# Optimization experiments

Hardware: AMD Instinct MI355X
Metric: run time of the kernel (lower is better)

Reference implementation:

```python
import jax, jax.numpy as jnp
import numpy as np

B, D_IN, D_H = 8192, 1024, 1024

def setup_inputs() -> dict:
    key = jax.random.key(0)
    ks = jax.random.split(key, 20)
    s_in = 1.0 / np.sqrt(D_IN)
    s_h = 1.0 / np.sqrt(D_H)
    inp = {
        'input': jax.random.normal(ks[0], (B, D_IN), jnp.float32),
        'h_0': jax.random.normal(ks[1], (B, D_H), jnp.float32),
        'c_0': jax.random.normal(ks[2], (B, D_H), jnp.float32),
    }
    names = ['i', 'f', 'g', 'o']
    for idx, g in enumerate(names):
        inp[f'W_{g}_i2h'] = jax.random.uniform(ks[3 + 4 * idx], (D_H, D_IN), jnp.float32, -s_in, s_in)
        inp[f'b_{g}_i2h'] = jax.random.uniform(ks[4 + 4 * idx], (D_H,), jnp.float32, -s_in, s_in)
        inp[f'W_{g}_h2h'] = jax.random.uniform(ks[5 + 4 * idx], (D_H, D_H), jnp.float32, -s_h, s_h)
        inp[f'b_{g}_h2h'] = jax.random.uniform(ks[6 + 4 * idx], (D_H,), jnp.float32, -s_h, s_h)
    return inp


def reference(input, h_0, c_0,
              W_i_i2h, b_i_i2h, W_i_h2h, b_i_h2h,
              W_f_i2h, b_f_i2h, W_f_h2h, b_f_h2h,
              W_g_i2h, b_g_i2h, W_g_h2h, b_g_h2h,
              W_o_i2h, b_o_i2h, W_o_h2h, b_o_h2h):
    # pre-activations: x @ W_i2h^T + b + h @ W_h2h^T + b  (Linear uses y = x W^T + b)
    def lin(x, W, b):
        return x @ W.T + b
    it = jax.nn.sigmoid(lin(input, W_i_i2h, b_i_i2h) + lin(h_0, W_i_h2h, b_i_h2h))
    ft = jax.nn.sigmoid(lin(input, W_f_i2h, b_f_i2h) + lin(h_0, W_f_h2h, b_f_h2h))
    ot = jax.nn.sigmoid(lin(input, W_o_i2h, b_o_i2h) + lin(h_0, W_o_h2h, b_o_h2h))
    gt = jnp.tanh(lin(input, W_g_i2h, b_g_i2h) + lin(h_0, W_g_h2h, b_g_h2h))
    ct = ft * c_0 + it * gt
    output = ot * jnp.tanh(ct)
    return (output, ct)
```

## Files before the change

### kernel.cpp

```cpp
#include <hip/hip_runtime.h>
#include <cstdint>

typedef __attribute__((ext_vector_type(8))) short bf16x8;
typedef __attribute__((ext_vector_type(4))) float f32x4;
typedef __attribute__((ext_vector_type(8))) unsigned short u16x8;

typedef __attribute__((address_space(1))) unsigned int gu32_t;
typedef __attribute__((address_space(3))) unsigned int lu32_t;

#define BATCH 8192
#define DIN 1024
#define DH 1024
#define KD 2048
#define ND 4096

__device__ __forceinline__ unsigned short f2bf(float f) {
    union { float f; unsigned int u; } v; v.f = f;
    unsigned int u = v.u;
    u += 0x7fffu + ((u >> 16) & 1u);
    return (unsigned short)(u >> 16);
}
__device__ __forceinline__ float sigmoidf_(float x) {
    return 1.0f / (1.0f + __expf(-x));
}
__device__ __forceinline__ float tanhf_(float x) {
    float xc = fminf(fmaxf(x, -15.0f), 15.0f);
    float e2 = __expf(2.0f * xc);
    return (e2 - 1.0f) / (e2 + 1.0f);
}

__global__ void __launch_bounds__(256) convert_all(
        const float* __restrict__ x, const float* __restrict__ h,
        const float* __restrict__ Wii, const float* __restrict__ Wih,
        const float* __restrict__ Wfi, const float* __restrict__ Wfh,
        const float* __restrict__ Wgi, const float* __restrict__ Wgh,
        const float* __restrict__ Woi, const float* __restrict__ Woh,
        const float* __restrict__ bii, const float* __restrict__ bih,
        const float* __restrict__ bfi, const float* __restrict__ bfh,
        const float* __restrict__ bgi, const float* __restrict__ bgh,
        const float* __restrict__ boi, const float* __restrict__ boh,
        unsigned short* __restrict__ A, unsigned short* __restrict__ B,
        float* __restrict__ bsum) {
    const int t = blockIdx.x * 256 + threadIdx.x;
    if (t < 2097152) {
        const int64_t off = (int64_t)t * 8;
        const int row = (int)(off >> 11);
        const int k = (int)(off & 2047);
        const float* src = (k < DIN) ? (x + (int64_t)row * DIN + k)
                                     : (h + (int64_t)row * DH + (k - DIN));
        f32x4 v0 = *(const f32x4*)src;
        f32x4 v1 = *(const f32x4*)(src + 4);
        u16x8 o;
        o[0] = f2bf(v0[0]); o[1] = f2bf(v0[1]); o[2] = f2bf(v0[2]); o[3] = f2bf(v0[3]);
        o[4] = f2bf(v1[0]); o[5] = f2bf(v1[1]); o[6] = f2bf(v1[2]); o[7] = f2bf(v1[3]);
        *(u16x8*)(A + off) = o;
    } else if (t < 3145728) {
        const int tb = t - 2097152;
        const int64_t off = (int64_t)tb * 8;
        const int brow = (int)(off >> 11);
        const int k = (int)(off & 2047);
        const int gate = brow & 3;
        const int n = brow >> 2;
        const float* Wi2h = (gate == 0) ? Wii : (gate == 1) ? Wfi : (gate == 2) ? Wgi : Woi;
        const float* Wh2h = (gate == 0) ? Wih : (gate == 1) ? Wfh : (gate == 2) ? Wgh : Woh;
        const float* src = (k < 1024) ? (Wi2h + (int64_t)n * 1024 + k)
                                      : (Wh2h + (int64_t)n * 1024 + (k - 1024));
        f32x4 v0 = *(const f32x4*)src;
        f32x4 v1 = *(const f32x4*)(src + 4);
        u16x8 o;
        o[0] = f2bf(v0[0]); o[1] = f2bf(v0[1]); o[2] = f2bf(v0[2]); o[3] = f2bf(v0[3]);
        o[4] = f2bf(v1[0]); o[5] = f2bf(v1[1]); o[6] = f2bf(v1[2]); o[7] = f2bf(v1[3]);
        *(u16x8*)(B + off) = o;
    } else {
        const int b = t - 3145728;
#pragma unroll
        for (int i = 0; i < 8; ++i) {
            const int e = b * 8 + i;
            const int n = e >> 2;
            const int g = e & 3;
            const float* bi = (g == 0) ? bii : (g == 1) ? bfi : (g == 2) ? bgi : boi;
            const float* bh = (g == 0) ? bih : (g == 1) ? bfh : (g == 2) ? bgh : boh;
            bsum[e] = bi[n] + bh[n];
        }
    }
}

__global__ void __launch_bounds__(256) gemm_lstm(
        const unsigned short* __restrict__ A,
        const unsigned short* __restrict__ Bw,
        const float* __restrict__ c0,
        const float* __restrict__ bsum,
        float* __restrict__ out) {
    __shared__ __align__(16) unsigned short ldsA[128 * 32];
    __shared__ __align__(16) unsigned short ldsB[128 * 32];
    __shared__ __align__(16) float preLds[64][128];

    const int bid = blockIdx.x;
    const int swz = ((bid & 7) << 8) | (bid >> 3);
    const int bm = swz >> 5;
    const int bn = swz & 31;
    const int t = threadIdx.x;
    const int lane = t & 63;
    const int wave = t >> 6;
    const int wm = (wave >> 1) << 6;
    const int wn = (wave & 1) << 6;

    f32x4 acc[4][4];
#pragma unroll
    for (int m = 0; m < 4; ++m)
#pragma unroll
        for (int n = 0; n < 4; ++n)
            acc[m][n] = (f32x4){0.f, 0.f, 0.f, 0.f};

    const int c0i = t;
    const int c1i = t + 256;
    const int64_t aOff0 = (int64_t)(bm * 128 + (c0i >> 2)) * KD + ((c0i & 3) << 3);
    const int64_t aOff1 = (int64_t)(bm * 128 + (c1i >> 2)) * KD + ((c1i & 3) << 3);
    const int64_t bOff0 = (int64_t)(bn * 128 + (c0i >> 2)) * KD + ((c0i & 3) << 3);
    const int64_t bOff1 = (int64_t)(bn * 128 + (c1i >> 2)) * KD + ((c1i & 3) << 3);
    unsigned short* lA0 = &ldsA[wave * 512];
    unsigned short* lA1 = &ldsA[2048 + wave * 512];
    unsigned short* lB0 = &ldsB[wave * 512];
    unsigned short* lB1 = &ldsB[2048 + wave * 512];

    const int r = lane & 15;
    const int kq = (lane >> 4) << 3;

    for (int k0 = 0; k0 < KD; k0 += 32) {
        __syncthreads();
        __builtin_amdgcn_global_load_lds((const gu32_t*)(A + aOff0 + k0), (lu32_t*)lA0, 16, 0, 0);
        __builtin_amdgcn_global_load_lds((const gu32_t*)(A + aOff1 + k0), (lu32_t*)lA1, 16, 0, 0);
        __builtin_amdgcn_global_load_lds((const gu32_t*)(Bw + bOff0 + k0), (lu32_t*)lB0, 16, 0, 0);
        __builtin_amdgcn_global_load_lds((const gu32_t*)(Bw + bOff1 + k0), (lu32_t*)lB1, 16, 0, 0);
        __syncthreads();

        bf16x8 af[4], bfr[4];
#pragma unroll
        for (int m = 0; m < 4; ++m)
            af[m] = *(const bf16x8*)&ldsA[(wm + m * 16 + r) * 32 + kq];
#pragma unroll
        for (int n = 0; n < 4; ++n)
            bfr[n] = *(const bf16x8*)&ldsB[(wn + n * 16 + r) * 32 + kq];
#pragma unroll
        for (int m = 0; m < 4; ++m)
#pragma unroll
            for (int n = 0; n < 4; ++n)
                acc[m][n] = __builtin_amdgcn_mfma_f32_16x16x32_bf16(af[m], bfr[n], acc[m][n], 0, 0, 0);
    }

    f32x4 bs[4];
#pragma unroll
    for (int i = 0; i < 4; ++i)
        bs[i] = *(const f32x4*)&bsum[bn * 128 + (t & 7) * 16 + i * 4];

    const int rq = (lane >> 4) << 2;

#pragma unroll
    for (int c = 0; c < 2; ++c) {
        __syncthreads();
        if (wm == c * 64) {
#pragma unroll
            for (int m = 0; m < 4; ++m)
#pragma unroll
                for (int n = 0; n < 4; ++n)
#pragma unroll
                    for (int j = 0; j < 4; ++j)
                        preLds[m * 16 + rq + j][wn + n * 16 + r] = acc[m][n][j];
        }
        __syncthreads();
#pragma unroll
        for (int p = 0; p < 2; ++p) {
            const int lr = p * 32 + (t >> 3);
            const int R = bm * 128 + c * 64 + lr;
            f32x4 pr[4];
#pragma unroll
            for (int i = 0; i < 4; ++i)
                pr[i] = *(const f32x4*)&preLds[lr][(t & 7) * 16 + i * 4];
            const int64_t eo = (int64_t)R * DH + bn * 32 + (t & 7) * 4;
            f32x4 cv = *(const f32x4*)&c0[eo];
            f32x4 hv, ctv;
#pragma unroll
            for (int j = 0; j < 4; ++j) {
                float it = sigmoidf_(pr[j][0] + bs[j][0]);
                float ft = sigmoidf_(pr[j][1] + bs[j][1]);
                float gt = tanhf_(pr[j][2] + bs[j][2]);
                float ot = sigmoidf_(pr[j][3] + bs[j][3]);
                float ct = ft * cv[j] + it * gt;
                ctv[j] = ct;
                hv[j] = ot * tanhf_(ct);
            }
            *(f32x4*)&out[eo] = hv;
            *(f32x4*)&out[(int64_t)BATCH * DH + eo] = ctv;
        }
    }
}

extern "C" void kernel_launch(void* const* d_in, const int* in_sizes, int n_in,
                              void* d_out, int out_size, void* d_ws, size_t ws_size,
                              hipStream_t stream) {
    const float* x   = (const float*)d_in[0];
    const float* h0  = (const float*)d_in[1];
    const float* c0  = (const float*)d_in[2];
    const float* Wii = (const float*)d_in[3];
    const float* bii = (const float*)d_in[4];
    const float* Wih = (const float*)d_in[5];
    const float* bih = (const float*)d_in[6];
    const float* Wfi = (const float*)d_in[7];
    const float* bfi = (const float*)d_in[8];
    const float* Wfh = (const float*)d_in[9];
    const float* bfh = (const float*)d_in[10];
    const float* Wgi = (const float*)d_in[11];
    const float* bgi = (const float*)d_in[12];
    const float* Wgh = (const float*)d_in[13];
    const float* bgh = (const float*)d_in[14];
    const float* Woi = (const float*)d_in[15];
    const float* boi = (const float*)d_in[16];
    const float* Woh = (const float*)d_in[17];
    const float* boh = (const float*)d_in[18];

    unsigned short* A  = (unsigned short*)d_ws;
    unsigned short* Bw = A + (size_t)BATCH * KD;
    float* bsum = (float*)(Bw + (size_t)ND * KD);
    float* out = (float*)d_out;

    convert_all<<<12290, 256, 0, stream>>>(x, h0,
        Wii, Wih, Wfi, Wfh, Wgi, Wgh, Woi, Woh,
        bii, bih, bfi, bfh, bgi, bgh, boi, boh,
        A, Bw, bsum);
    gemm_lstm<<<2048, 256, 0, stream>>>(A, Bw, c0, bsum, out);
}
```

Baseline: 406.5 us.

## Use 256x256 tiles, 4-stage LDS pipeline, and XOR-swizzled shared memory in LSTM GEMM

The GEMM now uses 256x256 block tiles with 8 waves (512 threads) and a 4-buffer LDS ring. Global-to-LDS loads are issued three k-steps ahead, with explicit vmcnt waits and a single barrier per step, so memory latency overlaps with MFMA work. LDS reads and the epilogue staging buffer use an XOR swizzle to cut bank conflicts, and MFMA sections raise wave priority with s_setprio. The larger tiles improve data reuse per loaded byte. In exchange there are fewer blocks (512), higher register pressure from 32 accumulators per thread, and 128KB of LDS per block.

```diff
diff --git a/kernel.cpp b/kernel.cpp
--- a/kernel.cpp
+++ b/kernel.cpp
@@ -27,6 +27,9 @@
     float xc = fminf(fmaxf(x, -15.0f), 15.0f);
     float e2 = __expf(2.0f * xc);
     return (e2 - 1.0f) / (e2 + 1.0f);
+}
+__device__ __forceinline__ int fswz(int r) {
+    return ((r & 3) << 4) ^ ((r & 4) << 3);
 }
 
 __global__ void __launch_bounds__(256) convert_all(
@@ -85,113 +88,148 @@
     }
 }
 
-__global__ void __launch_bounds__(256) gemm_lstm(
+__global__ void __launch_bounds__(512, 2) gemm_lstm(
         const unsigned short* __restrict__ A,
         const unsigned short* __restrict__ Bw,
-        const float* __restrict__ c0,
+        const float* __restrict__ c0p,
         const float* __restrict__ bsum,
-        float* __restrict__ out) {
-    __shared__ __align__(16) unsigned short ldsA[128 * 32];
-    __shared__ __align__(16) unsigned short ldsB[128 * 32];
-    __shared__ __align__(16) float preLds[64][128];
+        float* __restrict__ outp) {
+    __shared__ __align__(16) unsigned short lds[4][16384];
 
     const int bid = blockIdx.x;
-    const int swz = ((bid & 7) << 8) | (bid >> 3);
-    const int bm = swz >> 5;
-    const int bn = swz & 31;
+    const int swz = ((bid & 7) << 6) | (bid >> 3);
+    const int bm = swz & 31;
+    const int bn = swz >> 5;
     const int t = threadIdx.x;
     const int lane = t & 63;
     const int wave = t >> 6;
-    const int wm = (wave >> 1) << 6;
-    const int wn = (wave & 1) << 6;
-
-    f32x4 acc[4][4];
-#pragma unroll
-    for (int m = 0; m < 4; ++m)
+    const int wm = wave >> 2;
+    const int wn = wave & 3;
+
+    f32x4 acc[8][4];
+#pragma unroll
+    for (int m = 0; m < 8; ++m)
 #pragma unroll
         for (int n = 0; n < 4; ++n)
             acc[m][n] = (f32x4){0.f, 0.f, 0.f, 0.f};
 
-    const int c0i = t;
-    const int c1i = t + 256;
-    const int64_t aOff0 = (int64_t)(bm * 128 + (c0i >> 2)) * KD + ((c0i & 3) << 3);
-    const int64_t aOff1 = (int64_t)(bm * 128 + (c1i >> 2)) * KD + ((c1i & 3) << 3);
-    const int64_t bOff0 = (int64_t)(bn * 128 + (c0i >> 2)) * KD + ((c0i & 3) << 3);
-    const int64_t bOff1 = (int64_t)(bn * 128 + (c1i >> 2)) * KD + ((c1i & 3) << 3);
-    unsigned short* lA0 = &ldsA[wave * 512];
-    unsigned short* lA1 = &ldsA[2048 + wave * 512];
-    unsigned short* lB0 = &ldsB[wave * 512];
-    unsigned short* lB1 = &ldsB[2048 + wave * 512];
-
-    const int r = lane & 15;
-    const int kq = (lane >> 4) << 3;
-
-    for (int k0 = 0; k0 < KD; k0 += 32) {
+    const int crow = t >> 2;
+    const int kb = ((t & 3) << 4) ^ fswz(crow & 7);
+    const unsigned short* aS0 = A  + (size_t)(bm * 256 + crow) * KD + (kb >> 1);
+    const unsigned short* aS1 = aS0 + (size_t)128 * KD;
+    const unsigned short* bS0 = Bw + (size_t)(bn * 256 + crow) * KD + (kb >> 1);
+    const unsigned short* bS1 = bS0 + (size_t)128 * KD;
+    const int ldsDst = wave * 512;
+
+    const int r15 = lane & 15;
+    const int rdk = ((((lane >> 4) << 4) ^ fswz(r15 & 7)) >> 1);
+    const int aoff = r15 * 32 + rdk;
+    const int aRowBase = (wm * 128) * 32;
+    const int bRowBase = 8192 + (wn * 64) * 32;
+
+#pragma unroll
+    for (int pt = 0; pt < 3; ++pt) {
+        unsigned short* dA = &lds[pt][ldsDst];
+        unsigned short* dB = &lds[pt][8192 + ldsDst];
+        __builtin_amdgcn_global_load_lds((const gu32_t*)(aS0 + pt * 32), (lu32_t*)dA, 16, 0, 0);
+        __builtin_amdgcn_global_load_lds((const gu32_t*)(aS1 + pt * 32), (lu32_t*)(dA + 4096), 16, 0, 0);
+        __builtin_amdgcn_global_load_lds((const gu32_t*)(bS0 + pt * 32), (lu32_t*)dB, 16, 0, 0);
+        __builtin_amdgcn_global_load_lds((const gu32_t*)(bS1 + pt * 32), (lu32_t*)(dB + 4096), 16, 0, 0);
+    }
+    asm volatile("s_waitcnt vmcnt(8)" ::: "memory");
+    __builtin_amdgcn_sched_barrier(0);
+    __builtin_amdgcn_s_barrier();
+    __builtin_amdgcn_sched_barrier(0);
+
+    for (int tt = 0; tt < 16; ++tt) {
+#pragma unroll
+        for (int q = 0; q < 4; ++q) {
+            const int t64 = tt * 4 + q;
+            if (t64 < 61) {
+                const int b3 = (q + 3) & 3;
+                unsigned short* dA = &lds[b3][ldsDst];
+                unsigned short* dB = &lds[b3][8192 + ldsDst];
+                const size_t ko = (size_t)(t64 + 3) * 32;
+                __builtin_amdgcn_global_load_lds((const gu32_t*)(aS0 + ko), (lu32_t*)dA, 16, 0, 0);
+                __builtin_amdgcn_global_load_lds((const gu32_t*)(aS1 + ko), (lu32_t*)(dA + 4096), 16, 0, 0);
+                __builtin_amdgcn_global_load_lds((const gu32_t*)(bS0 + ko), (lu32_t*)dB, 16, 0, 0);
+                __builtin_amdgcn_global_load_lds((const gu32_t*)(bS1 + ko), (lu32_t*)(dB + 4096), 16, 0, 0);
+            }
+            const unsigned short* aB = &lds[q][aRowBase + aoff];
+            const unsigned short* bB = &lds[q][bRowBase + aoff];
+            bf16x8 af[8], bf4[4];
+#pragma unroll
+            for (int m = 0; m < 8; ++m) af[m] = *(const bf16x8*)(aB + m * 512);
+#pragma unroll
+            for (int n = 0; n < 4; ++n) bf4[n] = *(const bf16x8*)(bB + n * 512);
+            __builtin_amdgcn_s_setprio(1);
+#pragma unroll
+            for (int m = 0; m < 8; ++m)
+#pragma unroll
+                for (int n = 0; n < 4; ++n)
+                    acc[m][n] = __builtin_amdgcn_mfma_f32_16x16x32_bf16(af[m], bf4[n], acc[m][n], 0, 0, 0);
+            __builtin_amdgcn_s_setprio(0);
+            if (t64 < 61)       asm volatile("s_waitcnt vmcnt(8)" ::: "memory");
+            else if (t64 == 61) asm volatile("s_waitcnt vmcnt(4)" ::: "memory");
+            else if (t64 == 62) asm volatile("s_waitcnt vmcnt(0)" ::: "memory");
+            if (t64 < 63) {
+                __builtin_amdgcn_sched_barrier(0);
+                __builtin_amdgcn_s_barrier();
+                __builtin_amdgcn_sched_barrier(0);
+            }
+        }
+    }
+
+    float* pre = (float*)&lds[0][0];
+    const int lr = t >> 3;
+    const int cg = t & 7;
+    const int rswz = (lr & 7) << 2;
+#pragma unroll
+    for (int c = 0; c < 4; ++c) {
         __syncthreads();
-        __builtin_amdgcn_global_load_lds((const gu32_t*)(A + aOff0 + k0), (lu32_t*)lA0, 16, 0, 0);
-        __builtin_amdgcn_global_load_lds((const gu32_t*)(A + aOff1 + k0), (lu32_t*)lA1, 16, 0, 0);
-        __builtin_amdgcn_global_load_lds((const gu32_t*)(Bw + bOff0 + k0), (lu32_t*)lB0, 16, 0, 0);
-        __builtin_amdgcn_global_load_lds((const gu32_t*)(Bw + bOff1 + k0), (lu32_t*)lB1, 16, 0, 0);
+        if (wm == (c >> 1)) {
+#pragma unroll
+            for (int mm = 0; mm < 4; ++mm) {
+                const int m = (c & 1) * 4 + mm;
+#pragma unroll
+                for (int n = 0; n < 4; ++n) {
+                    const int col = wn * 64 + n * 16 + r15;
+#pragma unroll
+                    for (int j = 0; j < 4; ++j) {
+                        const int rw = mm * 16 + ((lane >> 4) << 2) + j;
+                        pre[rw * 256 + (col ^ ((rw & 7) << 2))] = acc[m][n][j];
+                    }
+                }
+            }
+        }
         __syncthreads();
-
-        bf16x8 af[4], bfr[4];
-#pragma unroll
-        for (int m = 0; m < 4; ++m)
-            af[m] = *(const bf16x8*)&ldsA[(wm + m * 16 + r) * 32 + kq];
-#pragma unroll
-        for (int n = 0; n < 4; ++n)
-            bfr[n] = *(const bf16x8*)&ldsB[(wn + n * 16 + r) * 32 + kq];
-#pragma unroll
-        for (int m = 0; m < 4; ++m)
-#pragma unroll
-            for (int n = 0; n < 4; ++n)
-                acc[m][n] = __builtin_amdgcn_mfma_f32_16x16x32_bf16(af[m], bfr[n], acc[m][n], 0, 0, 0);
-    }
-
-    f32x4 bs[4];
-#pragma unroll
-    for (int i = 0; i < 4; ++i)
-        bs[i] = *(const f32x4*)&bsum[bn * 128 + (t & 7) * 16 + i * 4];
-
-    const int rq = (lane >> 4) << 2;
-
-#pragma unroll
-    for (int c = 0; c < 2; ++c) {
-        __syncthreads();
-        if (wm == c * 64) {
-#pragma unroll
-            for (int m = 0; m < 4; ++m)
-#pragma unroll
-                for (int n = 0; n < 4; ++n)
-#pragma unroll
-                    for (int j = 0; j < 4; ++j)
-                        preLds[m * 16 + rq + j][wn + n * 16 + r] = acc[m][n][j];
-        }
-        __syncthreads();
-#pragma unroll
-        for (int p = 0; p < 2; ++p) {
-            const int lr = p * 32 + (t >> 3);
-            const int R = bm * 128 + c * 64 + lr;
-            f32x4 pr[4];
-#pragma unroll
-            for (int i = 0; i < 4; ++i)
-                pr[i] = *(const f32x4*)&preLds[lr][(t & 7) * 16 + i * 4];
-            const int64_t eo = (int64_t)R * DH + bn * 32 + (t & 7) * 4;
-            f32x4 cv = *(const f32x4*)&c0[eo];
-            f32x4 hv, ctv;
-#pragma unroll
-            for (int j = 0; j < 4; ++j) {
-                float it = sigmoidf_(pr[j][0] + bs[j][0]);
-                float ft = sigmoidf_(pr[j][1] + bs[j][1]);
-                float gt = tanhf_(pr[j][2] + bs[j][2]);
-                float ot = sigmoidf_(pr[j][3] + bs[j][3]);
-                float ct = ft * cv[j] + it * gt;
-                ctv[j] = ct;
-                hv[j] = ot * tanhf_(ct);
-            }
-            *(f32x4*)&out[eo] = hv;
-            *(f32x4*)&out[(int64_t)BATCH * DH + eo] = ctv;
-        }
+        const int R = bm * 256 + c * 64 + lr;
+        const int64_t eo = (int64_t)R * DH + bn * 64 + cg * 8;
+        f32x4 cp0 = *(const f32x4*)&c0p[eo];
+        f32x4 cp1 = *(const f32x4*)&c0p[eo + 4];
+        float hbuf[8], cbuf[8];
+#pragma unroll
+        for (int g8 = 0; g8 < 8; ++g8) {
+            const int colf = cg * 32 + g8 * 4;
+            f32x4 pr = *(const f32x4*)&pre[lr * 256 + (colf ^ rswz)];
+            f32x4 bs = *(const f32x4*)&bsum[bn * 256 + colf];
+            float it = sigmoidf_(pr[0] + bs[0]);
+            float ft = sigmoidf_(pr[1] + bs[1]);
+            float gt = tanhf_(pr[2] + bs[2]);
+            float ot = sigmoidf_(pr[3] + bs[3]);
+            float cprev = (g8 < 4) ? cp0[g8 & 3] : cp1[g8 & 3];
+            float ct = ft * cprev + it * gt;
+            cbuf[g8] = ct;
+            hbuf[g8] = ot * tanhf_(ct);
+        }
+        f32x4 h0v = {hbuf[0], hbuf[1], hbuf[2], hbuf[3]};
+        f32x4 h1v = {hbuf[4], hbuf[5], hbuf[6], hbuf[7]};
+        f32x4 c0v = {cbuf[0], cbuf[1], cbuf[2], cbuf[3]};
+        f32x4 c1v = {cbuf[4], cbuf[5], cbuf[6], cbuf[7]};
+        *(f32x4*)&outp[eo] = h0v;
+        *(f32x4*)&outp[eo + 4] = h1v;
+        *(f32x4*)&outp[(int64_t)BATCH * DH + eo] = c0v;
+        *(f32x4*)&outp[(int64_t)BATCH * DH + eo + 4] = c1v;
     }
 }
 
@@ -227,5 +265,5 @@
         Wii, Wih, Wfi, Wfh, Wgi, Wgh, Woi, Woh,
         bii, bih, bfi, bfh, bgi, bgh, boi, boh,
         A, Bw, bsum);
-    gemm_lstm<<<2048, 256, 0, stream>>>(A, Bw, c0, bsum, out);
-}
+    gemm_lstm<<<512, 512, 0, stream>>>(A, Bw, c0, bsum, out);
+}
```

Result: faster. 334.2 us (-17.8%).
